# Optimization experiments

Hardware: AMD Instinct MI355X
Metric: run time of the kernel (lower is better)

Reference implementation:

```python
import jax, jax.numpy as jnp
import numpy as np

H_IMG, W_IMG = 2160, 3840


def _avgpool3x3(x):
    # AvgPool2d(3, stride=1, padding=1), count_include_pad=True -> divide by 9 always
    s = jax.lax.reduce_window(x, 0.0, jax.lax.add, (3, 3, 1), (1, 1, 1), 'SAME')
    return s / 9.0


def setup_inputs() -> dict:
    key = jax.random.key(0)
    k1, k2, k3, k4 = jax.random.split(key, 4)
    depth = jax.random.uniform(k1, (H_IMG, W_IMG), jnp.float32) * 4.0 + 0.5
    rgb = jax.random.uniform(k2, (H_IMG, W_IMG, 3), jnp.float32)
    mask = jax.random.randint(k3, (H_IMG, W_IMG), 0, 2, jnp.int32)
    l = jax.random.normal(k4, (9, 3), jnp.float32) * 0.3
    fx = fy = 3000.0
    cx, cy = W_IMG / 2.0, H_IMG / 2.0
    CameraParam = jnp.array([[fx, 0.0, cx], [0.0, fy, cy], [0.0, 0.0, 1.0]], jnp.float32)
    return {'depth': depth, 'rgb': rgb, 'mask': mask, 'l': l, 'CameraParam': CameraParam}


def reference(depth, rgb, mask, l, CameraParam):
    nrows, ncols = depth.shape
    imask = mask > 0                      # [H, W] bool
    m3 = imask[..., None]                 # [H, W, 1]

    # Homogeneous pixel grid -> back-projected rays (precomputed in torch __init__)
    yy, xx = jnp.meshgrid(jnp.arange(nrows, dtype=jnp.float32),
                          jnp.arange(ncols, dtype=jnp.float32), indexing='ij')
    p2d = jnp.stack([xx, yy, jnp.ones_like(xx)], axis=-1)      # [H, W, 3]
    Kinv = jnp.linalg.inv(CameraParam)
    p3d = jnp.einsum('ij,hwj->hwi', Kinv, p2d)                 # [H, W, 3]

    # Depth -> 3D points, shifted neighbors (zero-padded at borders)
    p = p3d * depth[..., None]                                 # [H, W, 3]
    pl = jnp.pad(p[:, 1:, :], ((0, 0), (0, 1), (0, 0)))        # right neighbor
    pu = jnp.pad(p[1:, :, :], ((0, 1), (0, 0), (0, 0)))        # down neighbor

    n = jnp.cross(pl - p, pu - p)                              # [H, W, 3]
    norm = jnp.linalg.norm(n, axis=-1, keepdims=True)
    n = n / jnp.maximum(norm, 1e-12)                           # F.normalize

    nx, ny, nz = n[..., 0], n[..., 1], n[..., 2]
    ones = jnp.ones_like(nx)
    Hsh = jnp.stack([ones, ny, nz, nx, nx * ny, ny * nz,
                     -nx * nx - ny * ny + 2.0 * nz * nz,
                     nz * nx, nx * nx - ny * ny], axis=-1)     # [H, W, 9]
    B = jnp.einsum('hwk,kc->hwc', Hsh, l)                      # [H, W, 3]

    # Scatter into full image: zero outside mask (matches render_img[imask] = B)
    render = jnp.where(m3, B, 0.0)
    render_mean = jax.lax.stop_gradient(_avgpool3x3(render))   # render_img.detach()
    rgbmean = _avgpool3x3(jax.lax.stop_gradient(rgb))          # rgb.detach()

    diff = (render - render_mean) - (rgb - rgbmean)
    cnt = jnp.sum(imask).astype(jnp.float32) * 3.0             # MSE over masked elems
    loss = jnp.sum(jnp.where(m3, diff * diff, 0.0)) / cnt
    return loss
```

## Files before the change

### kernel.cpp

```cpp
#include <hip/hip_runtime.h>
#include <math.h>

#define H_IMG 2160
#define W_IMG 3840
#define SPAN 120
#define NSX 32
#define HS 8
#define WPB 4
#define NSY 68
#define NBLOCKS (NSX * NSY)
#define NBINS 2048

__global__ __launch_bounds__(256, 4) void shading_main(
    const float* __restrict__ depth,
    const float* __restrict__ rgb,
    const int*   __restrict__ mask,
    const float* __restrict__ lmat,
    const float* __restrict__ K,
    float* __restrict__ accum,
    int direct)
{
    const int tid  = threadIdx.x;
    const int lane = tid & 63;
    const int wv   = tid >> 6;
    const int sx   = blockIdx.x;
    const int x0   = sx * SPAN;
    const int y0   = blockIdx.y * (WPB * HS) + wv * HS;
    const int colBase  = x0 + 2 * lane;
    const int colBase3 = 3 * colBase;
    const bool fullIn = (colBase + 1) < W_IMG;

    const float m00 = K[0], m01 = K[1], m02 = K[2];
    const float m10 = K[3], m11 = K[4], m12 = K[5];
    const float m20 = K[6], m21 = K[7], m22 = K[8];
    const float det = m00*(m11*m22 - m12*m21)
                    - m01*(m10*m22 - m12*m20)
                    + m02*(m10*m21 - m11*m20);
    const float id  = 1.0f / det;
    const float i00 = (m11*m22 - m12*m21) * id;
    const float i01 = (m02*m21 - m01*m22) * id;
    const float i02 = (m01*m12 - m02*m11) * id;
    const float i10 = (m12*m20 - m10*m22) * id;
    const float i11 = (m00*m22 - m02*m20) * id;
    const float i12 = (m02*m10 - m00*m12) * id;
    const float i20 = (m10*m21 - m11*m20) * id;
    const float i21 = (m01*m20 - m00*m21) * id;
    const float i22 = (m00*m11 - m01*m10) * id;

    float L[27];
    #pragma unroll
    for (int i = 0; i < 27; ++i) L[i] = lmat[i];

    float wout[2];
    #pragma unroll
    for (int k = 0; k < 2; ++k) {
        const int c  = colBase + k;
        const int lc = 2 * lane + k;
        const bool v = (c < W_IMG) && (lc <= SPAN) && (lc >= 1 || sx == 0);
        wout[k] = v ? 1.0f : 0.0f;
    }
    const float qm1s = (lane == 0) ? 0.0f : 1.0f;

    float rx = fmaf(i00, (float)colBase, fmaf(i01, (float)(y0 - 1), i02));
    float ry = fmaf(i10, (float)colBase, fmaf(i11, (float)(y0 - 1), i12));
    float rz = fmaf(i20, (float)colBase, fmaf(i21, (float)(y0 - 1), i22));

    const float2 Z2 = make_float2(0.f, 0.f);

    float2 dC = Z2, dN = Z2;
    float2 raC = Z2, rbC = Z2, rcC = Z2;
    int2   mC  = make_int2(0, 0);
    if (fullIn) {
        if (y0 > 0 && (y0 - 1) < H_IMG) {
            const size_t pix = (size_t)(y0 - 1) * W_IMG + colBase;
            dC  = *(const float2*)(depth + pix);
            raC = *(const float2*)(rgb + (size_t)(y0 - 1) * (3 * W_IMG) + colBase3);
            rbC = *(const float2*)(rgb + (size_t)(y0 - 1) * (3 * W_IMG) + colBase3 + 2);
            rcC = *(const float2*)(rgb + (size_t)(y0 - 1) * (3 * W_IMG) + colBase3 + 4);
            mC  = *(const int2*)(mask + pix);
        }
        if (y0 < H_IMG)
            dN = *(const float2*)(depth + (size_t)y0 * W_IMG + colBase);
    }

    float sA0[2] = {0,0}, sA1[2] = {0,0}, sA2[2] = {0,0};
    float sB0[2] = {0,0}, sB1[2] = {0,0}, sB2[2] = {0,0};
    float qB0[2] = {0,0}, qB1[2] = {0,0}, qB2[2] = {0,0};
    float wB[2]  = {0,0};
    float accS = 0.f, accC = 0.f;

    #pragma unroll 1
    for (int j = 0; j < HS + 2; ++j) {
        const int h = y0 - 1 + j;

        float2 dP = Z2, raN = Z2, rbN = Z2, rcN = Z2;
        int2   mN = make_int2(0, 0);
        if (fullIn) {
            if (h + 2 < H_IMG)
                dP = *(const float2*)(depth + (size_t)(h + 2) * W_IMG + colBase);
            if (h + 1 < H_IMG) {
                const float* rr = rgb + (size_t)(h + 1) * (3 * W_IMG);
                raN = *(const float2*)(rr + colBase3);
                rbN = *(const float2*)(rr + colBase3 + 2);
                rcN = *(const float2*)(rr + colBase3 + 4);
                mN  = *(const int2*)(mask + (size_t)(h + 1) * W_IMG + colBase);
            }
        }

        const float dcv[2] = {dC.x, dC.y};
        const float dnv[2] = {dN.x, dN.y};
        const float rrv[6] = {raC.x, raC.y, rbC.x, rbC.y, rcC.x, rcC.y};
        const int   mmv[2] = {mC.x, mC.y};
        const float dcR = __shfl_down(dC.x, 1, 64);

        float qC0[2], qC1[2], qC2[2], wC[2];
        float rxk = rx, ryk = ry, rzk = rz;
        #pragma unroll
        for (int k = 0; k < 2; ++k) {
            const float d0 = dcv[k];
            const float dR = (k == 0) ? dcv[1] : dcR;
            const float dD = dnv[k];
            const float px = rxk * d0, py = ryk * d0, pz = rzk * d0;
            const float ax = (rxk + i00) * dR - px;
            const float ay = (ryk + i10) * dR - py;
            const float az = (rzk + i20) * dR - pz;
            const float bx = (rxk + i01) * dD - px;
            const float by = (ryk + i11) * dD - py;
            const float bz = (rzk + i21) * dD - pz;
            float nx = ay*bz - az*by;
            float ny = az*bx - ax*bz;
            float nz = ax*by - ay*bx;
            const float nn  = nx*nx + ny*ny + nz*nz;
            const float inr = __builtin_amdgcn_rsqf(fmaxf(nn, 1e-24f));
            nx *= inr; ny *= inr; nz *= inr;
            const float h4 = nx*ny, h5 = ny*nz, h7 = nz*nx;
            const float nx2 = nx*nx, ny2 = ny*ny, nz2 = nz*nz;
            const float h6 = 2.f*nz2 - nx2 - ny2;
            const float h8 = nx2 - ny2;
            const float B0 = L[0] + ny*L[3] + nz*L[6] + nx*L[9]  + h4*L[12] + h5*L[15] + h6*L[18] + h7*L[21] + h8*L[24];
            const float B1 = L[1] + ny*L[4] + nz*L[7] + nx*L[10] + h4*L[13] + h5*L[16] + h6*L[19] + h7*L[22] + h8*L[25];
            const float B2 = L[2] + ny*L[5] + nz*L[8] + nx*L[11] + h4*L[14] + h5*L[17] + h6*L[20] + h7*L[23] + h8*L[26];
            const float m  = (mmv[k] > 0) ? 1.0f : 0.0f;
            qC0[k] = fmaf(m, B0, -rrv[3*k + 0]);
            qC1[k] = fmaf(m, B1, -rrv[3*k + 1]);
            qC2[k] = fmaf(m, B2, -rrv[3*k + 2]);
            wC[k]  = m * wout[k];
            rxk += i00; ryk += i10; rzk += i20;
        }

        float sC0[2], sC1[2], sC2[2];
        {
            const float a0 = __shfl_up(qC0[1], 1, 64) * qm1s;
            const float a1 = __shfl_up(qC1[1], 1, 64) * qm1s;
            const float a2 = __shfl_up(qC2[1], 1, 64) * qm1s;
            const float p0 = __shfl_down(qC0[0], 1, 64);
            const float p1 = __shfl_down(qC1[0], 1, 64);
            const float p2 = __shfl_down(qC2[0], 1, 64);

            const float t0 = qC0[0] + qC0[1];
            sC0[0] = a0 + t0;
            sC0[1] = t0 + p0;
            const float t1 = qC1[0] + qC1[1];
            sC1[0] = a1 + t1;
            sC1[1] = t1 + p1;
            const float t2 = qC2[0] + qC2[1];
            sC2[0] = a2 + t2;
            sC2[1] = t2 + p2;
        }

        if (j >= 2) {
            #pragma unroll
            for (int k = 0; k < 2; ++k) {
                const float v0 = sA0[k] + sB0[k] + sC0[k];
                const float v1 = sA1[k] + sB1[k] + sC1[k];
                const float v2 = sA2[k] + sB2[k] + sC2[k];
                const float d0 = fmaf(v0, -(1.f/9.f), qB0[k]);
                const float d1 = fmaf(v1, -(1.f/9.f), qB1[k]);
                const float d2 = fmaf(v2, -(1.f/9.f), qB2[k]);
                const float w  = wB[k];
                accS = fmaf(w, d0*d0 + d1*d1 + d2*d2, accS);
                accC += w;
            }
        }

        #pragma unroll
        for (int k = 0; k < 2; ++k) {
            sA0[k] = sB0[k]; sA1[k] = sB1[k]; sA2[k] = sB2[k];
            sB0[k] = sC0[k]; sB1[k] = sC1[k]; sB2[k] = sC2[k];
            qB0[k] = qC0[k]; qB1[k] = qC1[k]; qB2[k] = qC2[k];
            wB[k]  = wC[k];
        }
        dC = dN; dN = dP;
        raC = raN; rbC = rbN; rcC = rcN; mC = mN;
        rx += i01; ry += i11; rz += i21;
    }

    #pragma unroll
    for (int off = 32; off > 0; off >>= 1) {
        accS += __shfl_down(accS, off, 64);
        accC += __shfl_down(accC, off, 64);
    }
    __shared__ float sS[WPB], sC[WPB];
    if (lane == 0) { sS[wv] = accS; sC[wv] = accC; }
    __syncthreads();
    if (tid == 0) {
        const float ts = sS[0] + sS[1] + sS[2] + sS[3];
        const float tc = sC[0] + sC[1] + sC[2] + sC[3];
        const int bid = blockIdx.y * gridDim.x + blockIdx.x;
        if (direct) {
            accum[2*bid + 0] = ts;
            accum[2*bid + 1] = tc;
        } else {
            const int bin = bid & (NBINS - 1);
            atomicAdd(&accum[2*bin + 0], ts);
            atomicAdd(&accum[2*bin + 1], tc);
        }
    }
}

__global__ __launch_bounds__(256) void finalize_kernel(
    const float* __restrict__ part, int n, float* __restrict__ out)
{
    const int tid = threadIdx.x;
    float s = 0.f, c = 0.f;
    for (int i = tid; i < n; i += 256) {
        s += part[2*i + 0];
        c += part[2*i + 1];
    }
    #pragma unroll
    for (int off = 32; off > 0; off >>= 1) {
        s += __shfl_down(s, off, 64);
        c += __shfl_down(c, off, 64);
    }
    __shared__ float sS[4], sC[4];
    const int wid = tid >> 6, lane = tid & 63;
    if (lane == 0) { sS[wid] = s; sC[wid] = c; }
    __syncthreads();
    if (tid == 0) {
        const float ts = sS[0] + sS[1] + sS[2] + sS[3];
        const float tc = sC[0] + sC[1] + sC[2] + sC[3];
        out[0] = ts / (3.0f * tc);
    }
}

extern "C" void kernel_launch(void* const* d_in, const int* in_sizes, int n_in,
                              void* d_out, int out_size, void* d_ws, size_t ws_size,
                              hipStream_t stream) {
    const float* depth = (const float*)d_in[0];
    const float* rgb   = (const float*)d_in[1];
    const int*   mask  = (const int*)  d_in[2];
    const float* lmat  = (const float*)d_in[3];
    const float* K     = (const float*)d_in[4];
    float* accum = (float*)d_ws;
    float* out   = (float*)d_out;

    const dim3 grid(NSX, NSY);

    if (ws_size >= (size_t)NBLOCKS * 2 * sizeof(float)) {
        shading_main<<<grid, 256, 0, stream>>>(depth, rgb, mask, lmat, K, accum, 1);
        finalize_kernel<<<1, 256, 0, stream>>>(accum, NBLOCKS, out);
    } else {
        hipMemsetAsync(accum, 0, NBINS * 2 * sizeof(float), stream);
        shading_main<<<grid, 256, 0, stream>>>(depth, rgb, mask, lmat, K, accum, 0);
        finalize_kernel<<<1, 256, 0, stream>>>(accum, NBINS, out);
    }
}
```

Baseline: 213.1 us.

## Stream interior rows through a per-wave LDS ring using async global-to-LDS loads

For interior blocks, each wave now prefetches depth, mask and RGB rows into a four-slot LDS ring with global_load_lds, keeping up to three rows in flight. Explicit vmcnt waits replace the register double-buffered global loads. The last column strip is shifted left so every lane loads in bounds, which removes the fullIn predicate, and edge rows keep a simplified register path. This trades about 48 KB of LDS per block and hand-managed waitcnt ordering for deeper memory latency hiding, and the LDS footprint may limit occupancy.

```diff
diff --git a/kernel.cpp b/kernel.cpp
--- a/kernel.cpp
+++ b/kernel.cpp
@@ -10,6 +10,8 @@
 #define NSY 68
 #define NBLOCKS (NSX * NSY)
 #define NBINS 2048
+#define RING 4
+#define SLOT_B 3072
 
 __global__ __launch_bounds__(256, 4) void shading_main(
     const float* __restrict__ depth,
@@ -20,15 +22,17 @@
     float* __restrict__ accum,
     int direct)
 {
+    __shared__ __align__(16) unsigned char ringmem[WPB][RING][SLOT_B];
+    __shared__ float sS[WPB], sC[WPB];
+
     const int tid  = threadIdx.x;
     const int lane = tid & 63;
     const int wv   = tid >> 6;
     const int sx   = blockIdx.x;
-    const int x0   = sx * SPAN;
+    const int x0   = min(sx * SPAN, W_IMG - 128);
     const int y0   = blockIdx.y * (WPB * HS) + wv * HS;
     const int colBase  = x0 + 2 * lane;
     const int colBase3 = 3 * colBase;
-    const bool fullIn = (colBase + 1) < W_IMG;
 
     const float m00 = K[0], m01 = K[1], m02 = K[2];
     const float m10 = K[3], m11 = K[4], m12 = K[5];
@@ -54,9 +58,9 @@
     float wout[2];
     #pragma unroll
     for (int k = 0; k < 2; ++k) {
-        const int c  = colBase + k;
-        const int lc = 2 * lane + k;
-        const bool v = (c < W_IMG) && (lc <= SPAN) && (lc >= 1 || sx == 0);
+        const int c   = colBase + k;
+        const int rel = c - sx * SPAN;
+        const bool v  = (c < W_IMG) && (rel <= SPAN) && (rel >= 1 || sx == 0);
         wout[k] = v ? 1.0f : 0.0f;
     }
     const float qm1s = (lane == 0) ? 0.0f : 1.0f;
@@ -66,22 +70,6 @@
     float rz = fmaf(i20, (float)colBase, fmaf(i21, (float)(y0 - 1), i22));
 
     const float2 Z2 = make_float2(0.f, 0.f);
-
-    float2 dC = Z2, dN = Z2;
-    float2 raC = Z2, rbC = Z2, rcC = Z2;
-    int2   mC  = make_int2(0, 0);
-    if (fullIn) {
-        if (y0 > 0 && (y0 - 1) < H_IMG) {
-            const size_t pix = (size_t)(y0 - 1) * W_IMG + colBase;
-            dC  = *(const float2*)(depth + pix);
-            raC = *(const float2*)(rgb + (size_t)(y0 - 1) * (3 * W_IMG) + colBase3);
-            rbC = *(const float2*)(rgb + (size_t)(y0 - 1) * (3 * W_IMG) + colBase3 + 2);
-            rcC = *(const float2*)(rgb + (size_t)(y0 - 1) * (3 * W_IMG) + colBase3 + 4);
-            mC  = *(const int2*)(mask + pix);
-        }
-        if (y0 < H_IMG)
-            dN = *(const float2*)(depth + (size_t)y0 * W_IMG + colBase);
-    }
 
     float sA0[2] = {0,0}, sA1[2] = {0,0}, sA2[2] = {0,0};
     float sB0[2] = {0,0}, sB1[2] = {0,0}, sB2[2] = {0,0};
@@ -89,110 +77,255 @@
     float wB[2]  = {0,0};
     float accS = 0.f, accC = 0.f;
 
-    #pragma unroll 1
-    for (int j = 0; j < HS + 2; ++j) {
-        const int h = y0 - 1 + j;
-
-        float2 dP = Z2, raN = Z2, rbN = Z2, rcN = Z2;
-        int2   mN = make_int2(0, 0);
-        if (fullIn) {
-            if (h + 2 < H_IMG)
-                dP = *(const float2*)(depth + (size_t)(h + 2) * W_IMG + colBase);
-            if (h + 1 < H_IMG) {
-                const float* rr = rgb + (size_t)(h + 1) * (3 * W_IMG);
-                raN = *(const float2*)(rr + colBase3);
-                rbN = *(const float2*)(rr + colBase3 + 2);
-                rcN = *(const float2*)(rr + colBase3 + 4);
-                mN  = *(const int2*)(mask + (size_t)(h + 1) * W_IMG + colBase);
-            }
+    const bool interior = (y0 >= 8) && (y0 + 12 < H_IMG);
+
+    if (interior) {
+        unsigned char* const rb = &ringmem[wv][0][0];
+        const int offD = 8 * lane;
+        const int offM = 512 + 8 * lane;
+        const int offR = 1024 + 24 * lane;
+
+        const char* gDM = (lane < 32)
+            ? (const char*)(depth + (size_t)(y0 - 1) * W_IMG + x0 + 4 * lane)
+            : (const char*)(mask  + (size_t)(y0 - 1) * W_IMG + x0 + 4 * (lane - 32));
+        const char* gRA = (const char*)(rgb + (size_t)(y0 - 1) * (3 * W_IMG) + 3 * x0)
+                        + 16 * lane;
+        const char* gRB = gRA + 1024;
+
+#define STAGE(S) do {                                                          \
+        unsigned char* lb_ = rb + (S) * SLOT_B;                                \
+        __builtin_amdgcn_global_load_lds((const void*)gDM, (void*)lb_, 16, 0, 0); \
+        __builtin_amdgcn_global_load_lds((const void*)gRA, (void*)(lb_ + 1024), 16, 0, 0); \
+        __builtin_amdgcn_global_load_lds((const void*)gRB, (void*)(lb_ + 2048), 16, 0, 0); \
+        gDM += 15360; gRA += 46080; gRB += 46080;                              \
+    } while (0)
+
+        STAGE(0); STAGE(1); STAGE(2);
+        int s_st = 3, s_cu = 0, s_nx = 1;
+
+#define BODYI(WN, STG, EM) do {                                                \
+    if (STG) { STAGE(s_st); }                                                  \
+    asm volatile("s_waitcnt vmcnt(" #WN ")" ::: "memory");                     \
+    __builtin_amdgcn_sched_barrier(0);                                         \
+    const unsigned char* lc_ = rb + s_cu * SLOT_B;                             \
+    const unsigned char* ln_ = rb + s_nx * SLOT_B;                             \
+    const float2 dCv = *(const float2*)(lc_ + offD);                           \
+    const float  dRr = *(const float*)(lc_ + offD + 8);                        \
+    const float2 dNv = *(const float2*)(ln_ + offD);                           \
+    const float2 r0v = *(const float2*)(lc_ + offR);                           \
+    const float2 r1v = *(const float2*)(lc_ + offR + 8);                       \
+    const float2 r2v = *(const float2*)(lc_ + offR + 16);                      \
+    const int2   mv  = *(const int2*)(lc_ + offM);                             \
+    \
+    const float dcR = (lane == 63) ? dCv.y : dRr;                              \
+    const float dcv[2] = {dCv.x, dCv.y};                                       \
+    const float dnv[2] = {dNv.x, dNv.y};                                       \
+    const float rrv[6] = {r0v.x, r0v.y, r1v.x, r1v.y, r2v.x, r2v.y};           \
+    const int   mmv[2] = {mv.x, mv.y};                                         \
+    float qC0[2], qC1[2], qC2[2], wC[2];                                       \
+    float rxk = rx, ryk = ry, rzk = rz;                                        \
+    _Pragma("unroll")                                                          \
+    for (int k = 0; k < 2; ++k) {                                              \
+        const float d0 = dcv[k];                                               \
+        const float dR = (k == 0) ? dcv[1] : dcR;                              \
+        const float dD = dnv[k];                                               \
+        const float px = rxk * d0, py = ryk * d0, pz = rzk * d0;               \
+        const float ax = (rxk + i00) * dR - px;                                \
+        const float ay = (ryk + i10) * dR - py;                                \
+        const float az = (rzk + i20) * dR - pz;                                \
+        const float bx = (rxk + i01) * dD - px;                                \
+        const float by = (ryk + i11) * dD - py;                                \
+        const float bz = (rzk + i21) * dD - pz;                                \
+        float nx = ay*bz - az*by;                                              \
+        float ny = az*bx - ax*bz;                                              \
+        float nz = ax*by - ay*bx;                                              \
+        const float nn  = nx*nx + ny*ny + nz*nz;                               \
+        const float inr = __builtin_amdgcn_rsqf(fmaxf(nn, 1e-24f));            \
+        nx *= inr; ny *= inr; nz *= inr;                                       \
+        const float h4 = nx*ny, h5 = ny*nz, h7 = nz*nx;                        \
+        const float nx2 = nx*nx, ny2 = ny*ny, nz2 = nz*nz;                     \
+        const float h6 = 2.f*nz2 - nx2 - ny2;                                  \
+        const float h8 = nx2 - ny2;                                            \
+        const float B0 = L[0] + ny*L[3] + nz*L[6] + nx*L[9]  + h4*L[12]        \
+                       + h5*L[15] + h6*L[18] + h7*L[21] + h8*L[24];            \
+        const float B1 = L[1] + ny*L[4] + nz*L[7] + nx*L[10] + h4*L[13]        \
+                       + h5*L[16] + h6*L[19] + h7*L[22] + h8*L[25];            \
+        const float B2 = L[2] + ny*L[5] + nz*L[8] + nx*L[11] + h4*L[14]        \
+                       + h5*L[17] + h6*L[20] + h7*L[23] + h8*L[26];            \
+        const float m  = (mmv[k] > 0) ? 1.0f : 0.0f;                           \
+        qC0[k] = fmaf(m, B0, -rrv[3*k + 0]);                                   \
+        qC1[k] = fmaf(m, B1, -rrv[3*k + 1]);                                   \
+        qC2[k] = fmaf(m, B2, -rrv[3*k + 2]);                                   \
+        wC[k]  = m * wout[k];                                                  \
+        rxk += i00; ryk += i10; rzk += i20;                                    \
+    }                                                                          \
+    float sC0[2], sC1[2], sC2[2];                                              \
+    {                                                                          \
+        const float a0 = __shfl_up(qC0[1], 1, 64) * qm1s;                      \
+        const float a1 = __shfl_up(qC1[1], 1, 64) * qm1s;                      \
+        const float a2 = __shfl_up(qC2[1], 1, 64) * qm1s;                      \
+        const float p0 = __shfl_down(qC0[0], 1, 64);                           \
+        const float p1 = __shfl_down(qC1[0], 1, 64);                           \
+        const float p2 = __shfl_down(qC2[0], 1, 64);                           \
+        const float t0 = qC0[0] + qC0[1];                                      \
+        sC0[0] = a0 + t0;  sC0[1] = t0 + p0;                                   \
+        const float t1 = qC1[0] + qC1[1];                                      \
+        sC1[0] = a1 + t1;  sC1[1] = t1 + p1;                                   \
+        const float t2 = qC2[0] + qC2[1];                                      \
+        sC2[0] = a2 + t2;  sC2[1] = t2 + p2;                                   \
+    }                                                                          \
+    if (EM) {                                                                  \
+        _Pragma("unroll")                                                      \
+        for (int k = 0; k < 2; ++k) {                                          \
+            const float v0 = sA0[k] + sB0[k] + sC0[k];                         \
+            const float v1 = sA1[k] + sB1[k] + sC1[k];                         \
+            const float v2 = sA2[k] + sB2[k] + sC2[k];                         \
+            const float e0 = fmaf(v0, -(1.f/9.f), qB0[k]);                     \
+            const float e1 = fmaf(v1, -(1.f/9.f), qB1[k]);                     \
+            const float e2 = fmaf(v2, -(1.f/9.f), qB2[k]);                     \
+            const float w  = wB[k];                                            \
+            const float t  = e0*e0 + e1*e1 + e2*e2;                            \
+            accS += (w > 0.f) ? t : 0.f;   \
+            accC += w;                                                         \
+        }                                                                      \
+    }                                                                          \
+    _Pragma("unroll")                                                          \
+    for (int k = 0; k < 2; ++k) {                                              \
+        sA0[k] = sB0[k]; sA1[k] = sB1[k]; sA2[k] = sB2[k];                     \
+        sB0[k] = sC0[k]; sB1[k] = sC1[k]; sB2[k] = sC2[k];                     \
+        qB0[k] = qC0[k]; qB1[k] = qC1[k]; qB2[k] = qC2[k];                     \
+        wB[k]  = wC[k];                                                        \
+    }                                                                          \
+    s_cu = s_nx;                                                               \
+    s_nx = (s_nx + 1) & (RING - 1);                                            \
+    s_st = (s_st + 1) & (RING - 1);                                            \
+    rx += i01; ry += i11; rz += i21;                                           \
+} while (0)
+
+        #pragma unroll 1
+        for (int j = 0; j < 8; ++j) {
+            const bool em = (j >= 2);
+            BODYI(6, 1, em);
         }
-
-        const float dcv[2] = {dC.x, dC.y};
-        const float dnv[2] = {dN.x, dN.y};
-        const float rrv[6] = {raC.x, raC.y, rbC.x, rbC.y, rcC.x, rcC.y};
-        const int   mmv[2] = {mC.x, mC.y};
-        const float dcR = __shfl_down(dC.x, 1, 64);
-
-        float qC0[2], qC1[2], qC2[2], wC[2];
-        float rxk = rx, ryk = ry, rzk = rz;
-        #pragma unroll
-        for (int k = 0; k < 2; ++k) {
-            const float d0 = dcv[k];
-            const float dR = (k == 0) ? dcv[1] : dcR;
-            const float dD = dnv[k];
-            const float px = rxk * d0, py = ryk * d0, pz = rzk * d0;
-            const float ax = (rxk + i00) * dR - px;
-            const float ay = (ryk + i10) * dR - py;
-            const float az = (rzk + i20) * dR - pz;
-            const float bx = (rxk + i01) * dD - px;
-            const float by = (ryk + i11) * dD - py;
-            const float bz = (rzk + i21) * dD - pz;
-            float nx = ay*bz - az*by;
-            float ny = az*bx - ax*bz;
-            float nz = ax*by - ay*bx;
-            const float nn  = nx*nx + ny*ny + nz*nz;
-            const float inr = __builtin_amdgcn_rsqf(fmaxf(nn, 1e-24f));
-            nx *= inr; ny *= inr; nz *= inr;
-            const float h4 = nx*ny, h5 = ny*nz, h7 = nz*nx;
-            const float nx2 = nx*nx, ny2 = ny*ny, nz2 = nz*nz;
-            const float h6 = 2.f*nz2 - nx2 - ny2;
-            const float h8 = nx2 - ny2;
-            const float B0 = L[0] + ny*L[3] + nz*L[6] + nx*L[9]  + h4*L[12] + h5*L[15] + h6*L[18] + h7*L[21] + h8*L[24];
-            const float B1 = L[1] + ny*L[4] + nz*L[7] + nx*L[10] + h4*L[13] + h5*L[16] + h6*L[19] + h7*L[22] + h8*L[25];
-            const float B2 = L[2] + ny*L[5] + nz*L[8] + nx*L[11] + h4*L[14] + h5*L[17] + h6*L[20] + h7*L[23] + h8*L[26];
-            const float m  = (mmv[k] > 0) ? 1.0f : 0.0f;
-            qC0[k] = fmaf(m, B0, -rrv[3*k + 0]);
-            qC1[k] = fmaf(m, B1, -rrv[3*k + 1]);
-            qC2[k] = fmaf(m, B2, -rrv[3*k + 2]);
-            wC[k]  = m * wout[k];
-            rxk += i00; ryk += i10; rzk += i20;
+        BODYI(3, 0, true);
+        BODYI(0, 0, true);
+#undef BODYI
+#undef STAGE
+    } else {
+        float2 dC = Z2, dN = Z2;
+        float2 raC = Z2, rbC = Z2, rcC = Z2;
+        int2   mC  = make_int2(0, 0);
+        if (y0 > 0 && (y0 - 1) < H_IMG) {
+            const size_t r = (size_t)(y0 - 1);
+            dC  = *(const float2*)(depth + r * W_IMG + colBase);
+            raC = *(const float2*)(rgb + r * (3 * W_IMG) + colBase3);
+            rbC = *(const float2*)(rgb + r * (3 * W_IMG) + colBase3 + 2);
+            rcC = *(const float2*)(rgb + r * (3 * W_IMG) + colBase3 + 4);
+            mC  = *(const int2*)(mask + r * W_IMG + colBase);
         }
-
-        float sC0[2], sC1[2], sC2[2];
-        {
-            const float a0 = __shfl_up(qC0[1], 1, 64) * qm1s;
-            const float a1 = __shfl_up(qC1[1], 1, 64) * qm1s;
-            const float a2 = __shfl_up(qC2[1], 1, 64) * qm1s;
-            const float p0 = __shfl_down(qC0[0], 1, 64);
-            const float p1 = __shfl_down(qC1[0], 1, 64);
-            const float p2 = __shfl_down(qC2[0], 1, 64);
-
-            const float t0 = qC0[0] + qC0[1];
-            sC0[0] = a0 + t0;
-            sC0[1] = t0 + p0;
-            const float t1 = qC1[0] + qC1[1];
-            sC1[0] = a1 + t1;
-            sC1[1] = t1 + p1;
-            const float t2 = qC2[0] + qC2[1];
-            sC2[0] = a2 + t2;
-            sC2[1] = t2 + p2;
-        }
-
-        if (j >= 2) {
+        if (y0 < H_IMG)
+            dN = *(const float2*)(depth + (size_t)y0 * W_IMG + colBase);
+
+        const float* pfD = depth + (size_t)(y0 + 1) * W_IMG + colBase;
+        const float* pfR = rgb   + (size_t)y0 * (3 * W_IMG) + colBase3;
+        const int*   pfM = mask  + (size_t)y0 * W_IMG + colBase;
+
+        #pragma unroll 1
+        for (int j = 0; j < HS + 2; ++j) {
+            float2 dP = Z2, raN = Z2, rbN = Z2, rcN = Z2;
+            int2   mN = make_int2(0, 0);
+            if (y0 + 1 + j < H_IMG) dP = *(const float2*)pfD;
+            if (y0 + j < H_IMG) {
+                raN = *(const float2*)(pfR);
+                rbN = *(const float2*)(pfR + 2);
+                rcN = *(const float2*)(pfR + 4);
+                mN  = *(const int2*)(pfM);
+            }
+            pfD += W_IMG; pfR += 3 * W_IMG; pfM += W_IMG;
+
+            const float dcv[2] = {dC.x, dC.y};
+            const float dnv[2] = {dN.x, dN.y};
+            const float rrv[6] = {raC.x, raC.y, rbC.x, rbC.y, rcC.x, rcC.y};
+            const int   mmv[2] = {mC.x, mC.y};
+            const float dcR = __shfl_down(dC.x, 1, 64);
+
+            float qC0[2], qC1[2], qC2[2], wC[2];
+            float rxk = rx, ryk = ry, rzk = rz;
             #pragma unroll
             for (int k = 0; k < 2; ++k) {
-                const float v0 = sA0[k] + sB0[k] + sC0[k];
-                const float v1 = sA1[k] + sB1[k] + sC1[k];
-                const float v2 = sA2[k] + sB2[k] + sC2[k];
-                const float d0 = fmaf(v0, -(1.f/9.f), qB0[k]);
-                const float d1 = fmaf(v1, -(1.f/9.f), qB1[k]);
-                const float d2 = fmaf(v2, -(1.f/9.f), qB2[k]);
-                const float w  = wB[k];
-                accS = fmaf(w, d0*d0 + d1*d1 + d2*d2, accS);
-                accC += w;
-            }
+                const float d0 = dcv[k];
+                const float dR = (k == 0) ? dcv[1] : dcR;
+                const float dD = dnv[k];
+                const float px = rxk * d0, py = ryk * d0, pz = rzk * d0;
+                const float ax = (rxk + i00) * dR - px;
+                const float ay = (ryk + i10) * dR - py;
+                const float az = (rzk + i20) * dR - pz;
+                const float bx = (rxk + i01) * dD - px;
+                const float by = (ryk + i11) * dD - py;
+                const float bz = (rzk + i21) * dD - pz;
+                float nx = ay*bz - az*by;
+                float ny = az*bx - ax*bz;
+                float nz = ax*by - ay*bx;
+                const float nn  = nx*nx + ny*ny + nz*nz;
+                const float inr = __builtin_amdgcn_rsqf(fmaxf(nn, 1e-24f));
+                nx *= inr; ny *= inr; nz *= inr;
+                const float h4 = nx*ny, h5 = ny*nz, h7 = nz*nx;
+                const float nx2 = nx*nx, ny2 = ny*ny, nz2 = nz*nz;
+                const float h6 = 2.f*nz2 - nx2 - ny2;
+                const float h8 = nx2 - ny2;
+                const float B0 = L[0] + ny*L[3] + nz*L[6] + nx*L[9]  + h4*L[12] + h5*L[15] + h6*L[18] + h7*L[21] + h8*L[24];
+                const float B1 = L[1] + ny*L[4] + nz*L[7] + nx*L[10] + h4*L[13] + h5*L[16] + h6*L[19] + h7*L[22] + h8*L[25];
+                const float B2 = L[2] + ny*L[5] + nz*L[8] + nx*L[11] + h4*L[14] + h5*L[17] + h6*L[20] + h7*L[23] + h8*L[26];
+                const float m  = (mmv[k] > 0) ? 1.0f : 0.0f;
+                qC0[k] = fmaf(m, B0, -rrv[3*k + 0]);
+                qC1[k] = fmaf(m, B1, -rrv[3*k + 1]);
+                qC2[k] = fmaf(m, B2, -rrv[3*k + 2]);
+                wC[k]  = m * wout[k];
+                rxk += i00; ryk += i10; rzk += i20;
+            }
+
+            float sC0[2], sC1[2], sC2[2];
+            {
+                const float a0 = __shfl_up(qC0[1], 1, 64) * qm1s;
+                const float a1 = __shfl_up(qC1[1], 1, 64) * qm1s;
+                const float a2 = __shfl_up(qC2[1], 1, 64) * qm1s;
+                const float p0 = __shfl_down(qC0[0], 1, 64);
+                const float p1 = __shfl_down(qC1[0], 1, 64);
+                const float p2 = __shfl_down(qC2[0], 1, 64);
+                const float t0 = qC0[0] + qC0[1];
+                sC0[0] = a0 + t0;  sC0[1] = t0 + p0;
+                const float t1 = qC1[0] + qC1[1];
+                sC1[0] = a1 + t1;  sC1[1] = t1 + p1;
+                const float t2 = qC2[0] + qC2[1];
+                sC2[0] = a2 + t2;  sC2[1] = t2 + p2;
+            }
+
+            if (j >= 2) {
+                #pragma unroll
+                for (int k = 0; k < 2; ++k) {
+                    const float v0 = sA0[k] + sB0[k] + sC0[k];
+                    const float v1 = sA1[k] + sB1[k] + sC1[k];
+                    const float v2 = sA2[k] + sB2[k] + sC2[k];
+                    const float e0 = fmaf(v0, -(1.f/9.f), qB0[k]);
+                    const float e1 = fmaf(v1, -(1.f/9.f), qB1[k]);
+                    const float e2 = fmaf(v2, -(1.f/9.f), qB2[k]);
+                    const float w  = wB[k];
+                    accS = fmaf(w, e0*e0 + e1*e1 + e2*e2, accS);
+                    accC += w;
+                }
+            }
+
+            #pragma unroll
+            for (int k = 0; k < 2; ++k) {
+                sA0[k] = sB0[k]; sA1[k] = sB1[k]; sA2[k] = sB2[k];
+                sB0[k] = sC0[k]; sB1[k] = sC1[k]; sB2[k] = sC2[k];
+                qB0[k] = qC0[k]; qB1[k] = qC1[k]; qB2[k] = qC2[k];
+                wB[k]  = wC[k];
+            }
+            dC = dN; dN = dP;
+            raC = raN; rbC = rbN; rcC = rcN; mC = mN;
+            rx += i01; ry += i11; rz += i21;
         }
-
-        #pragma unroll
-        for (int k = 0; k < 2; ++k) {
-            sA0[k] = sB0[k]; sA1[k] = sB1[k]; sA2[k] = sB2[k];
-            sB0[k] = sC0[k]; sB1[k] = sC1[k]; sB2[k] = sC2[k];
-            qB0[k] = qC0[k]; qB1[k] = qC1[k]; qB2[k] = qC2[k];
-            wB[k]  = wC[k];
-        }
-        dC = dN; dN = dP;
-        raC = raN; rbC = rbN; rcC = rcN; mC = mN;
-        rx += i01; ry += i11; rz += i21;
     }
 
     #pragma unroll
@@ -200,7 +333,6 @@
         accS += __shfl_down(accS, off, 64);
         accC += __shfl_down(accC, off, 64);
     }
-    __shared__ float sS[WPB], sC[WPB];
     if (lane == 0) { sS[wv] = accS; sC[wv] = accC; }
     __syncthreads();
     if (tid == 0) {
```

Result: no change. 214.1 us (+0.5%).
